# Optimization experiments

Measured on AMD Instinct MI355X. Metric: run time of the kernel, lower is better.

## Reference

```python
import jax, jax.numpy as jnp
import numpy as np


def _conv1x1_relu(x, W, b):
    # x: (B, Cin, N, k), W: (Cout, Cin), b: (Cout,) -> (B, Cout, N, k)
    return jax.nn.relu(jnp.einsum('bcnk,oc->bonk', x, W) + b[None, :, None, None])


def _knn_idx(pc, k):
    # pc: (B, C, N). Mirrors torch: dis_mat = -||pi - pj||^2, topk (largest) -> nearest.
    G = jnp.einsum('bcn,bcm->bnm', pc, pc)            # (B, N, N)
    sq = jnp.sum(pc * pc, axis=1)                      # (B, N)
    neg_dist = 2.0 * G - sq[:, :, None] - sq[:, None, :]
    _, idx = jax.lax.top_k(neg_dist, k)                # (B, N, k) int32
    return idx


def _group_points(x, idx):
    # x: (B, C, N), idx: (B, N, k) -> (B, C, N, k); out[b,c,n,j] = x[b,c,idx[b,n,j]]
    B, C, N = x.shape
    k = idx.shape[-1]
    idx2 = jnp.broadcast_to(idx.reshape(B, 1, N * k), (B, C, N * k))
    return jnp.take_along_axis(x, idx2, axis=2).reshape(B, C, N, k)


def setup_inputs() -> dict:
    key = jax.random.key(0)
    ks = jax.random.split(key, 8)
    B, N, C, O, K = 8, 4096, 64, 64, 16
    s = 0.05
    return {
        'xyz': jax.random.normal(ks[0], (B, 3, N), dtype=jnp.float32),
        'fea': jax.random.normal(ks[1], (B, C, N), dtype=jnp.float32),
        'Wg1': jax.random.normal(ks[2], (O, 10), dtype=jnp.float32) * s,
        'bg1': jnp.zeros((O,), dtype=jnp.float32),
        'Wg2': jax.random.normal(ks[3], (O, O), dtype=jnp.float32) * s,
        'bg2': jnp.zeros((O,), dtype=jnp.float32),
        'Wf1': jax.random.normal(ks[4], (O, 2 * C), dtype=jnp.float32) * s,
        'bf1': jnp.zeros((O,), dtype=jnp.float32),
        'Wf2': jax.random.normal(ks[5], (O, O), dtype=jnp.float32) * s,
        'bf2': jnp.zeros((O,), dtype=jnp.float32),
        'Wf3': jax.random.normal(ks[6], (O, O), dtype=jnp.float32) * s,
        'bf3': jnp.zeros((O,), dtype=jnp.float32),
        'k': 16,
    }


def reference(xyz, fea, Wg1, bg1, Wg2, bg2, Wf1, bf1, Wf2, bf2, Wf3, bf3, k):
    idx = _knn_idx(fea, k)                             # (B, N, k)

    # get_edge_point: (B, 10, N, k)
    xyz_knn = _group_points(xyz, idx)                  # (B, 3, N, k)
    xyz_c = jnp.broadcast_to(xyz[:, :, :, None], xyz_knn.shape)
    xyz_r = xyz_c - xyz_knn
    xyz_d = jnp.sqrt(jnp.sum(xyz_r * xyz_r, axis=1, keepdims=True))
    geo = jnp.concatenate([xyz_d, xyz_c, xyz_knn, xyz_r], axis=1)

    # get_edge_feature: (B, 2C, N, k)
    fea_knn = _group_points(fea, idx)
    fea_c = jnp.broadcast_to(fea[:, :, :, None], fea_knn.shape)
    edge = jnp.concatenate([fea_c, fea_knn], axis=1)

    g = _conv1x1_relu(geo, Wg1, bg1)
    g = _conv1x1_relu(g, Wg2, bg2)

    f = _conv1x1_relu(edge, Wf1, bf1)
    f = _conv1x1_relu(f, Wf2, bf2)
    f = _conv1x1_relu(f, Wf3, bf3)

    out = jnp.max(g * f, axis=-1)                      # (B, O, N)
    return out
```

## Files before the change

kernel.cpp:

```cpp
#include <hip/hip_runtime.h>
#include <math.h>

#define NB 8
#define NPTS 4096
#define NCH 64
#define NOUT 64
#define KNN 16
#define HALFC 2048

#define GLOBAL_AS const __attribute__((address_space(1)))
#define LDS_AS __attribute__((address_space(3)))

#define WS_SQ  0
#define WS_PT  (NB*NPTS)
#define WS_QT  (WS_PT + NB*NPTS*64)
#define WS_IDX (WS_QT + NB*NPTS*64)

__global__ __launch_bounds__(256) void k_sq(const float* __restrict__ fea,
                                            float* __restrict__ sq) {
    int g = blockIdx.x * 256 + threadIdx.x;
    int b = g >> 12, n = g & 4095;
    const float* f = fea + (size_t)b * NCH * NPTS + n;
    float s = 0.f;
#pragma unroll
    for (int c = 0; c < NCH; ++c) s = fmaf(f[c * NPTS], f[c * NPTS], s);
    sq[g] = s;
}

__global__ __launch_bounds__(256, 4) void k_knn(const float* __restrict__ fea,
                                                const float* __restrict__ sq,
                                                float* __restrict__ vh,
                                                int* __restrict__ ih) {
    __shared__ __align__(16) float rowT[64][64];
    __shared__ __align__(16) float colT[64 * 64];

    const int b = blockIdx.z;
    const int half = blockIdx.y;
    const int n0 = blockIdx.x * 64;
    const int cbase = half * HALFC;
    const int tid = threadIdx.x;
    const int lane = tid & 63, w = tid >> 6;
    const int g = lane >> 4, p = lane & 15;
    const int rbase = w * 16 + g * 4;
    const float* feab = fea + (size_t)b * NCH * NPTS;

    auto stage = [&](int m0) {
#pragma unroll
        for (int i = 0; i < 4; ++i) {
            int k = w * 4 + i;
            int c = 4 * k + (lane >> 4);
            int j = (lane & 15) * 4;
            const float* gp = feab + c * NPTS + m0 + j;
            float* lp = &colT[k * 256];
            __builtin_amdgcn_global_load_lds((GLOBAL_AS void*)gp,
                                             (LDS_AS void*)lp, 16, 0, 0);
        }
    };

#pragma unroll
    for (int i = 0; i < 4; ++i) {
        int e = i * 1024 + tid * 4;
        int c = e >> 6, r = e & 63;
        *(float4*)&rowT[c][r] = *(const float4*)&feab[c * NPTS + n0 + r];
    }

    float lstv[4];
    int   lsti[4];
    float thr[4];
#pragma unroll
    for (int i = 0; i < 4; ++i) {
        lstv[i] = -3.0e38f; lsti[i] = 0; thr[i] = -3.0e38f;
    }

    auto ins = [&](int i, float vv, int col) {
        unsigned long long lt = __ballot(lstv[i] < vv);
        int pos = __popc((unsigned)((lt >> (g * 16)) & 0xFFFFu));
        int nv = __builtin_amdgcn_update_dpp(0, __float_as_int(lstv[i]),
                                             0x101, 0xF, 0xF, true);
        int ni = __builtin_amdgcn_update_dpp(0, lsti[i],
                                             0x101, 0xF, 0xF, true);
        if (p <= pos - 2)      { lstv[i] = __int_as_float(nv); lsti[i] = ni; }
        else if (p == pos - 1) { lstv[i] = vv; lsti[i] = col; }
    };

    stage(cbase);
    __syncthreads();

    for (int t = 0; t < 32; ++t) {
        const int m0 = cbase + t * 64;

        float4 sqc = *(const float4*)&sq[b * NPTS + m0 + p * 4];

        float acc[4][4] = {{0.f,0.f,0.f,0.f},{0.f,0.f,0.f,0.f},
                           {0.f,0.f,0.f,0.f},{0.f,0.f,0.f,0.f}};
#pragma unroll 8
        for (int c = 0; c < 64; ++c) {
            float4 rv = *(const float4*)&rowT[c][rbase];
            float4 cv = *(const float4*)&colT[c * 64 + p * 4];
            float rr[4] = {rv.x, rv.y, rv.z, rv.w};
            float cc[4] = {cv.x, cv.y, cv.z, cv.w};
#pragma unroll
            for (int ri = 0; ri < 4; ++ri)
#pragma unroll
                for (int ci = 0; ci < 4; ++ci)
                    acc[ri][ci] = fmaf(rr[ri], cc[ci], acc[ri][ci]);
        }

        __syncthreads();
        if (t < 31) stage(m0 + 64);

        float sqa[4] = {sqc.x, sqc.y, sqc.z, sqc.w};
#pragma unroll
        for (int i = 0; i < 4; ++i)
#pragma unroll
            for (int j = 0; j < 4; ++j)
                acc[i][j] = fmaf(2.f, acc[i][j], -sqa[j]);

#pragma unroll
        for (int i = 0; i < 4; ++i) {
            float v0 = acc[i][0], v1 = acc[i][1];
            float v2 = acc[i][2], v3 = acc[i][3];
            float vm = fmaxf(fmaxf(v0, v1), fmaxf(v2, v3));
            unsigned long long bal = __ballot(vm > thr[i]);
            unsigned mg = (unsigned)((bal >> (g * 16)) & 0xFFFFull);
            while (__any(mg != 0u)) {
                bool act = (mg != 0u);
                int srcp = act ? (__ffs(mg) - 1) : 0;
                mg &= (mg - 1u);
                int srcl = (g << 4) | srcp;
                float b0 = __shfl(v0, srcl);
                float b1 = __shfl(v1, srcl);
                float b2 = __shfl(v2, srcl);
                float b3 = __shfl(v3, srcl);
                if (act) {
                    int cb = m0 + srcp * 4;
                    if (b0 > thr[i]) ins(i, b0, cb + 0);
                    if (b1 > thr[i]) ins(i, b1, cb + 1);
                    if (b2 > thr[i]) ins(i, b2, cb + 2);
                    if (b3 > thr[i]) ins(i, b3, cb + 3);
                }
            }
            if (bal) thr[i] = __shfl(lstv[i], 0, 16);
        }
        __syncthreads();
    }

#pragma unroll
    for (int i = 0; i < 4; ++i) {
        int row = rbase + i;
        size_t base = ((size_t)(b * NPTS) + n0 + row) * 32 + half * 16;
        vh[base + (15 - p)] = lstv[i];
        ih[base + (15 - p)] = lsti[i];
    }
}

__global__ __launch_bounds__(256) void k_merge(const float* __restrict__ vh,
                                               const int* __restrict__ ih,
                                               int* __restrict__ idxout) {
    int row = blockIdx.x * 256 + threadIdx.x;
    const float* v = vh + (size_t)row * 32;
    const int* ii = ih + (size_t)row * 32;
    size_t ob = (size_t)row * KNN;
    int i0 = 0, i1 = 0;
#pragma unroll
    for (int j = 0; j < KNN; ++j) {
        float v0 = (i0 < 16) ? v[i0] : -3.4e38f;
        float v1 = (i1 < 16) ? v[16 + i1] : -3.4e38f;
        bool t0 = (v0 >= v1);
        idxout[ob + j] = t0 ? ii[i0] : ii[16 + i1];
        if (t0) ++i0; else ++i1;
    }
}

__global__ __launch_bounds__(256) void k_pq(const float* __restrict__ fea,
                                            const float* __restrict__ Wf1,
                                            const float* __restrict__ bf1,
                                            float* __restrict__ Pt,
                                            float* __restrict__ Qt) {
    __shared__ __align__(16) float feaT[64][64];
    __shared__ __align__(16) float WT[64][132];
    __shared__ float sb[64];

    const int b = blockIdx.y;
    const int n0 = blockIdx.x * 64;
    const int tid = threadIdx.x;
    const int to = tid & 15, tn = tid >> 4;
    const float* feab = fea + (size_t)b * NCH * NPTS;

#pragma unroll
    for (int i = 0; i < 4; ++i) {
        int e = i * 1024 + tid * 4;
        int c = e >> 6, nn = e & 63;
        *(float4*)&feaT[c][nn] = *(const float4*)&feab[c * NPTS + n0 + nn];
    }
#pragma unroll
    for (int i = 0; i < 8; ++i) {
        int g = tid * 32 + i * 4;
        int op = g >> 6, c = g & 63;
        const float* src = (op < 64) ? &Wf1[op * 128 + c]
                                     : &Wf1[(op - 64) * 128 + 64 + c];
        float4 w = *(const float4*)src;
        WT[c + 0][op] = w.x; WT[c + 1][op] = w.y;
        WT[c + 2][op] = w.z; WT[c + 3][op] = w.w;
    }
    if (tid < 64) sb[tid] = bf1[tid];
    __syncthreads();

    float acc[4][8];
#pragma unroll
    for (int ni = 0; ni < 4; ++ni)
#pragma unroll
        for (int oj = 0; oj < 8; ++oj) acc[ni][oj] = 0.f;

#pragma unroll 4
    for (int c = 0; c < 64; ++c) {
        float4 a  = *(const float4*)&feaT[c][tn * 4];
        float4 w0 = *(const float4*)&WT[c][to * 8];
        float4 w1 = *(const float4*)&WT[c][to * 8 + 4];
        float av[4] = {a.x, a.y, a.z, a.w};
        float wv[8] = {w0.x, w0.y, w0.z, w0.w, w1.x, w1.y, w1.z, w1.w};
#pragma unroll
        for (int ni = 0; ni < 4; ++ni)
#pragma unroll
            for (int oj = 0; oj < 8; ++oj)
                acc[ni][oj] = fmaf(av[ni], wv[oj], acc[ni][oj]);
    }

    const int opb = to * 8;
#pragma unroll
    for (int ni = 0; ni < 4; ++ni) {
        int n = n0 + tn * 4 + ni;
        size_t base = ((size_t)b * NPTS + n) * 64;
        if (opb < 64) {
            float4 o0, o1;
            o0.x = acc[ni][0] + sb[opb + 0]; o0.y = acc[ni][1] + sb[opb + 1];
            o0.z = acc[ni][2] + sb[opb + 2]; o0.w = acc[ni][3] + sb[opb + 3];
            o1.x = acc[ni][4] + sb[opb + 4]; o1.y = acc[ni][5] + sb[opb + 5];
            o1.z = acc[ni][6] + sb[opb + 6]; o1.w = acc[ni][7] + sb[opb + 7];
            *(float4*)&Pt[base + opb]     = o0;
            *(float4*)&Pt[base + opb + 4] = o1;
        } else {
            float4 o0, o1;
            o0.x = acc[ni][0]; o0.y = acc[ni][1]; o0.z = acc[ni][2]; o0.w = acc[ni][3];
            o1.x = acc[ni][4]; o1.y = acc[ni][5]; o1.z = acc[ni][6]; o1.w = acc[ni][7];
            *(float4*)&Qt[base + opb - 64]     = o0;
            *(float4*)&Qt[base + opb - 64 + 4] = o1;
        }
    }
}

__global__ __launch_bounds__(256) void k_mlp(
    const float* __restrict__ xyz,
    const float* __restrict__ Pt, const float* __restrict__ Qt,
    const int* __restrict__ knnidx,
    const float* __restrict__ Wg1, const float* __restrict__ bg1,
    const float* __restrict__ Wg2, const float* __restrict__ bg2,
    const float* __restrict__ Wf2, const float* __restrict__ bf2,
    const float* __restrict__ Wf3, const float* __restrict__ bf3,
    float* __restrict__ out) {
    __shared__ __align__(16) float bufX[64][68];
    __shared__ __align__(16) float bufY[64][68];
    __shared__ __align__(16) float Wbuf[64][68];
    __shared__ __align__(16) float scratch[1280];
    __shared__ float biasS[64];
    __shared__ int sidx[64];

    const int b = blockIdx.y;
    const int n0 = blockIdx.x * 4;
    const int tid = threadIdx.x;
    const int to = tid & 15, tp = tid >> 4;

    if (tid < 64)
        sidx[tid] = knnidx[((size_t)(b * NPTS + n0)) * KNN + tid];
    __syncthreads();

    {
        int pair = tid >> 2, q = tid & 3;
        int m = sidx[pair];
        int pt = pair >> 4;
        const float* pB = &Pt[((size_t)b * NPTS + n0 + pt) * 64];
        const float* qB = &Qt[((size_t)b * NPTS + m) * 64];
#pragma unroll
        for (int i = 0; i < 4; ++i) {
            int c0 = q * 16 + i * 4;
            float4 pv = *(const float4*)&pB[c0];
            float4 qv = *(const float4*)&qB[c0];
            bufX[c0 + 0][pair] = fmaxf(pv.x + qv.x, 0.f);
            bufX[c0 + 1][pair] = fmaxf(pv.y + qv.y, 0.f);
            bufX[c0 + 2][pair] = fmaxf(pv.z + qv.z, 0.f);
            bufX[c0 + 3][pair] = fmaxf(pv.w + qv.w, 0.f);
        }
    }
    if (tid < 64) {
        int pair = tid, pt = pair >> 4;
        int m = sidx[pair];
        const float* xb = xyz + (size_t)b * 3 * NPTS;
        float cx = xb[0 * NPTS + n0 + pt], cy = xb[1 * NPTS + n0 + pt], cz = xb[2 * NPTS + n0 + pt];
        float kx = xb[0 * NPTS + m], ky = xb[1 * NPTS + m], kz = xb[2 * NPTS + m];
        float rx = cx - kx, ry = cy - ky, rz = cz - kz;
        float d = sqrtf(rx * rx + ry * ry + rz * rz);
        scratch[0 * 68 + pair] = d;
        scratch[1 * 68 + pair] = cx; scratch[2 * 68 + pair] = cy; scratch[3 * 68 + pair] = cz;
        scratch[4 * 68 + pair] = kx; scratch[5 * 68 + pair] = ky; scratch[6 * 68 + pair] = kz;
        scratch[7 * 68 + pair] = rx; scratch[8 * 68 + pair] = ry; scratch[9 * 68 + pair] = rz;
    }

    auto stageW = [&](const float* W, const float* bv) {
#pragma unroll
        for (int i = 0; i < 4; ++i) {
            int g = tid * 16 + i * 4;
            int o = g >> 6, c = g & 63;
            float4 w = *(const float4*)&W[g];
            Wbuf[c + 0][o] = w.x; Wbuf[c + 1][o] = w.y;
            Wbuf[c + 2][o] = w.z; Wbuf[c + 3][o] = w.w;
        }
        if (tid < 64) biasS[tid] = bv[tid];
    };

    auto gemmPh = [&](const float* src, float* dst, int Kdim) {
        float acc[4][4] = {{0.f,0.f,0.f,0.f},{0.f,0.f,0.f,0.f},
                           {0.f,0.f,0.f,0.f},{0.f,0.f,0.f,0.f}};
#pragma unroll 2
        for (int c = 0; c < Kdim; ++c) {
            float4 w = *(const float4*)&Wbuf[c][to * 4];
            float4 a = *(const float4*)(src + c * 68 + tp * 4);
            float wr[4] = {w.x, w.y, w.z, w.w};
            float ar[4] = {a.x, a.y, a.z, a.w};
#pragma unroll
            for (int oi = 0; oi < 4; ++oi)
#pragma unroll
                for (int pj = 0; pj < 4; ++pj)
                    acc[oi][pj] = fmaf(wr[oi], ar[pj], acc[oi][pj]);
        }
#pragma unroll
        for (int oi = 0; oi < 4; ++oi) {
            float bo = biasS[to * 4 + oi];
            float4 o4;
            o4.x = fmaxf(acc[oi][0] + bo, 0.f);
            o4.y = fmaxf(acc[oi][1] + bo, 0.f);
            o4.z = fmaxf(acc[oi][2] + bo, 0.f);
            o4.w = fmaxf(acc[oi][3] + bo, 0.f);
            *(float4*)(dst + (to * 4 + oi) * 68 + tp * 4) = o4;
        }
    };

    stageW(Wf2, bf2);
    __syncthreads();
    gemmPh(&bufX[0][0], &bufY[0][0], 64);
    __syncthreads();
    stageW(Wf3, bf3);
    __syncthreads();
    gemmPh(&bufY[0][0], &bufX[0][0], 64);
    __syncthreads();
    {
        for (int e = tid; e < 640; e += 256) {
            int o = e / 10, c = e - o * 10;
            Wbuf[c][o] = Wg1[e];
        }
        if (tid < 64) biasS[tid] = bg1[tid];
    }
    __syncthreads();
    gemmPh(scratch, &bufY[0][0], 10);
    __syncthreads();
    stageW(Wg2, bg2);
    __syncthreads();
    {
        float acc[4][4] = {{0.f,0.f,0.f,0.f},{0.f,0.f,0.f,0.f},
                           {0.f,0.f,0.f,0.f},{0.f,0.f,0.f,0.f}};
#pragma unroll 2
        for (int c = 0; c < 64; ++c) {
            float4 w = *(const float4*)&Wbuf[c][to * 4];
            float4 a = *(const float4*)&bufY[c][tp * 4];
            float wr[4] = {w.x, w.y, w.z, w.w};
            float ar[4] = {a.x, a.y, a.z, a.w};
#pragma unroll
            for (int oi = 0; oi < 4; ++oi)
#pragma unroll
                for (int pj = 0; pj < 4; ++pj)
                    acc[oi][pj] = fmaf(wr[oi], ar[pj], acc[oi][pj]);
        }
#pragma unroll
        for (int oi = 0; oi < 4; ++oi) {
            int o = to * 4 + oi;
            float bo = biasS[o];
            float mx = -3.0e38f;
#pragma unroll
            for (int pj = 0; pj < 4; ++pj) {
                float g2v = fmaxf(acc[oi][pj] + bo, 0.f);
                float f3v = bufX[o][tp * 4 + pj];
                mx = fmaxf(mx, g2v * f3v);
            }
            scratch[o * 17 + tp] = mx;
        }
    }
    __syncthreads();
    {
        int o = tid & 63, pt = tid >> 6;
        float m0_ = scratch[o * 17 + pt * 4 + 0];
        float m1  = scratch[o * 17 + pt * 4 + 1];
        float m2  = scratch[o * 17 + pt * 4 + 2];
        float m3  = scratch[o * 17 + pt * 4 + 3];
        out[((size_t)b * 64 + o) * NPTS + n0 + pt] =
            fmaxf(fmaxf(m0_, m1), fmaxf(m2, m3));
    }
}

extern "C" void kernel_launch(void* const* d_in, const int* in_sizes, int n_in,
                              void* d_out, int out_size, void* d_ws, size_t ws_size,
                              hipStream_t stream) {
    const float* xyz = (const float*)d_in[0];
    const float* fea = (const float*)d_in[1];
    const float* Wg1 = (const float*)d_in[2];
    const float* bg1 = (const float*)d_in[3];
    const float* Wg2 = (const float*)d_in[4];
    const float* bg2 = (const float*)d_in[5];
    const float* Wf1 = (const float*)d_in[6];
    const float* bf1 = (const float*)d_in[7];
    const float* Wf2 = (const float*)d_in[8];
    const float* bf2 = (const float*)d_in[9];
    const float* Wf3 = (const float*)d_in[10];
    const float* bf3 = (const float*)d_in[11];
    float* out = (float*)d_out;
    float* ws = (float*)d_ws;

    float* sq = ws + WS_SQ;
    float* Pt = ws + WS_PT;
    float* Qt = ws + WS_QT;
    int* idxw = (int*)(ws + WS_IDX);
    float* vh = ws + WS_PT;
    int*   ih = (int*)(ws + WS_PT + NB * NPTS * 32);

    k_sq   <<<dim3(128),       dim3(256), 0, stream>>>(fea, sq);
    k_knn  <<<dim3(64, 2, 8),  dim3(256), 0, stream>>>(fea, sq, vh, ih);
    k_merge<<<dim3(128),       dim3(256), 0, stream>>>(vh, ih, idxw);
    k_pq   <<<dim3(64, 8),     dim3(256), 0, stream>>>(fea, Wf1, bf1, Pt, Qt);
    k_mlp  <<<dim3(1024, 8),   dim3(256), 0, stream>>>(xyz, Pt, Qt, idxw,
                                                       Wg1, bg1, Wg2, bg2,
                                                       Wf2, bf2, Wf3, bf3, out);
}
```

Before: 698.7 us.

## Drop column split in kNN; each block scans all columns for 32 rows

The kNN kernel no longer splits candidate columns into two halves followed by a merge kernel. Each block now handles 32 query rows over all 4096 candidates and writes final indices directly, so the k_merge launch and the intermediate value/index buffers go away. The grid size stays the same (1024 blocks), but each thread now owns 2 rows instead of 4. That halves register-tile reuse of each colT load, so arithmetic intensity on LDS drops while the number of staged column tiles per block doubles.

```diff
diff --git a/kernel.cpp b/kernel.cpp
--- a/kernel.cpp
+++ b/kernel.cpp
@@ -6,7 +6,6 @@
 #define NCH 64
 #define NOUT 64
 #define KNN 16
-#define HALFC 2048
 
 #define GLOBAL_AS const __attribute__((address_space(1)))
 #define LDS_AS __attribute__((address_space(3)))
@@ -29,19 +28,16 @@
 
 __global__ __launch_bounds__(256, 4) void k_knn(const float* __restrict__ fea,
                                                 const float* __restrict__ sq,
-                                                float* __restrict__ vh,
-                                                int* __restrict__ ih) {
-    __shared__ __align__(16) float rowT[64][64];
+                                                int* __restrict__ idxout) {
+    __shared__ __align__(16) float rowT[64][32];
     __shared__ __align__(16) float colT[64 * 64];
 
-    const int b = blockIdx.z;
-    const int half = blockIdx.y;
-    const int n0 = blockIdx.x * 64;
-    const int cbase = half * HALFC;
+    const int b = blockIdx.y;
+    const int n0 = blockIdx.x * 32;
     const int tid = threadIdx.x;
     const int lane = tid & 63, w = tid >> 6;
     const int g = lane >> 4, p = lane & 15;
-    const int rbase = w * 16 + g * 4;
+    const int rbase = w * 8 + g * 2;
     const float* feab = fea + (size_t)b * NCH * NPTS;
 
     auto stage = [&](int m0) {
@@ -58,17 +54,17 @@
     };
 
 #pragma unroll
-    for (int i = 0; i < 4; ++i) {
+    for (int i = 0; i < 2; ++i) {
         int e = i * 1024 + tid * 4;
-        int c = e >> 6, r = e & 63;
+        int c = e >> 5, r = e & 31;
         *(float4*)&rowT[c][r] = *(const float4*)&feab[c * NPTS + n0 + r];
     }
 
-    float lstv[4];
-    int   lsti[4];
-    float thr[4];
-#pragma unroll
-    for (int i = 0; i < 4; ++i) {
+    float lstv[2];
+    int   lsti[2];
+    float thr[2];
+#pragma unroll
+    for (int i = 0; i < 2; ++i) {
         lstv[i] = -3.0e38f; lsti[i] = 0; thr[i] = -3.0e38f;
     }
 
@@ -83,41 +79,39 @@
         else if (p == pos - 1) { lstv[i] = vv; lsti[i] = col; }
     };
 
-    stage(cbase);
-    __syncthreads();
-
-    for (int t = 0; t < 32; ++t) {
-        const int m0 = cbase + t * 64;
+    stage(0);
+    __syncthreads();
+
+    for (int t = 0; t < 64; ++t) {
+        const int m0 = t * 64;
 
         float4 sqc = *(const float4*)&sq[b * NPTS + m0 + p * 4];
 
-        float acc[4][4] = {{0.f,0.f,0.f,0.f},{0.f,0.f,0.f,0.f},
-                           {0.f,0.f,0.f,0.f},{0.f,0.f,0.f,0.f}};
+        float acc[2][4] = {{0.f,0.f,0.f,0.f},{0.f,0.f,0.f,0.f}};
 #pragma unroll 8
         for (int c = 0; c < 64; ++c) {
-            float4 rv = *(const float4*)&rowT[c][rbase];
+            float2 rv = *(const float2*)&rowT[c][rbase];
             float4 cv = *(const float4*)&colT[c * 64 + p * 4];
-            float rr[4] = {rv.x, rv.y, rv.z, rv.w};
             float cc[4] = {cv.x, cv.y, cv.z, cv.w};
 #pragma unroll
-            for (int ri = 0; ri < 4; ++ri)
-#pragma unroll
-                for (int ci = 0; ci < 4; ++ci)
-                    acc[ri][ci] = fmaf(rr[ri], cc[ci], acc[ri][ci]);
+            for (int ci = 0; ci < 4; ++ci) {
+                acc[0][ci] = fmaf(rv.x, cc[ci], acc[0][ci]);
+                acc[1][ci] = fmaf(rv.y, cc[ci], acc[1][ci]);
+            }
         }
 
         __syncthreads();
-        if (t < 31) stage(m0 + 64);
+        if (t < 63) stage(m0 + 64);
 
         float sqa[4] = {sqc.x, sqc.y, sqc.z, sqc.w};
 #pragma unroll
-        for (int i = 0; i < 4; ++i)
+        for (int i = 0; i < 2; ++i)
 #pragma unroll
             for (int j = 0; j < 4; ++j)
                 acc[i][j] = fmaf(2.f, acc[i][j], -sqa[j]);
 
 #pragma unroll
-        for (int i = 0; i < 4; ++i) {
+        for (int i = 0; i < 2; ++i) {
             float v0 = acc[i][0], v1 = acc[i][1];
             float v2 = acc[i][2], v3 = acc[i][3];
             float vm = fmaxf(fmaxf(v0, v1), fmaxf(v2, v3));
@@ -146,29 +140,9 @@
     }
 
 #pragma unroll
-    for (int i = 0; i < 4; ++i) {
+    for (int i = 0; i < 2; ++i) {
         int row = rbase + i;
-        size_t base = ((size_t)(b * NPTS) + n0 + row) * 32 + half * 16;
-        vh[base + (15 - p)] = lstv[i];
-        ih[base + (15 - p)] = lsti[i];
-    }
-}
-
-__global__ __launch_bounds__(256) void k_merge(const float* __restrict__ vh,
-                                               const int* __restrict__ ih,
-                                               int* __restrict__ idxout) {
-    int row = blockIdx.x * 256 + threadIdx.x;
-    const float* v = vh + (size_t)row * 32;
-    const int* ii = ih + (size_t)row * 32;
-    size_t ob = (size_t)row * KNN;
-    int i0 = 0, i1 = 0;
-#pragma unroll
-    for (int j = 0; j < KNN; ++j) {
-        float v0 = (i0 < 16) ? v[i0] : -3.4e38f;
-        float v1 = (i1 < 16) ? v[16 + i1] : -3.4e38f;
-        bool t0 = (v0 >= v1);
-        idxout[ob + j] = t0 ? ii[i0] : ii[16 + i1];
-        if (t0) ++i0; else ++i1;
+        idxout[((size_t)(b * NPTS) + n0 + row) * KNN + (15 - p)] = lsti[i];
     }
 }
 
@@ -427,14 +401,11 @@
     float* Pt = ws + WS_PT;
     float* Qt = ws + WS_QT;
     int* idxw = (int*)(ws + WS_IDX);
-    float* vh = ws + WS_PT;
-    int*   ih = (int*)(ws + WS_PT + NB * NPTS * 32);
-
-    k_sq   <<<dim3(128),       dim3(256), 0, stream>>>(fea, sq);
-    k_knn  <<<dim3(64, 2, 8),  dim3(256), 0, stream>>>(fea, sq, vh, ih);
-    k_merge<<<dim3(128),       dim3(256), 0, stream>>>(vh, ih, idxw);
-    k_pq   <<<dim3(64, 8),     dim3(256), 0, stream>>>(fea, Wf1, bf1, Pt, Qt);
-    k_mlp  <<<dim3(1024, 8),   dim3(256), 0, stream>>>(xyz, Pt, Qt, idxw,
-                                                       Wg1, bg1, Wg2, bg2,
-                                                       Wf2, bf2, Wf3, bf3, out);
+
+    k_sq  <<<dim3(128),      dim3(256), 0, stream>>>(fea, sq);
+    k_knn <<<dim3(128, 8),   dim3(256), 0, stream>>>(fea, sq, idxw);
+    k_pq  <<<dim3(64, 8),    dim3(256), 0, stream>>>(fea, Wf1, bf1, Pt, Qt);
+    k_mlp <<<dim3(1024, 8),  dim3(256), 0, stream>>>(xyz, Pt, Qt, idxw,
+                                                     Wg1, bg1, Wg2, bg2,
+                                                     Wf2, bf2, Wf3, bf3, out);
 }
```

New measurement: 673.5 us. 1.04x faster.
